# Optimization experiments

Hardware: AMD Instinct MI355X
Metric: run time of the kernel (lower is better)

## Reference

```python
import jax, jax.numpy as jnp
import numpy as np
import math

B, C, H, W = 64, 32, 80, 80
HEADS, HD = 8, 4
L = H * W
INV_PI = 1.0 / math.pi


def _conv2d(x, w, pad):
    return jax.lax.conv_general_dilated(x, w, (1, 1), pad, dimension_numbers=('NCHW', 'OIHW', 'NCHW'))


def _lin_angular(x, qkv_w, proj_w, proj_b, dconv_w):
    # x: (B, L, C) -> softmax-free angular linear attention
    qkv = (x @ qkv_w.T).reshape(B, L, 3, HEADS, HD).transpose(2, 0, 3, 1, 4)
    q, k, v = qkv[0], qkv[1], qkv[2]  # (B, HEADS, L, HD)
    q = q / jnp.linalg.norm(q, axis=-1, keepdims=True)
    k = k / jnp.linalg.norm(k, axis=-1, keepdims=True)
    # depthwise conv over L with kernel (9,1), one channel per head
    dconv_v = jax.lax.conv_general_dilated(v, dconv_w, (1, 1), ((4, 4), (0, 0)),
                                           feature_group_count=HEADS,
                                           dimension_numbers=('NCHW', 'OIHW', 'NCHW'))
    attn = jnp.einsum('bhld,bhle->bhde', k, v)  # (B,H,HD,HD)
    out = 0.5 * v + INV_PI * jnp.einsum('bhld,bhde->bhle', q, attn)
    out = out / jnp.linalg.norm(out, axis=-1, keepdims=True)
    out = out + dconv_v
    out = out.transpose(0, 2, 1, 3).reshape(B, L, C)
    return out @ proj_w.T + proj_b


def _xca(x, qkv_w, temp, proj_w, proj_b):
    # x: (B, L, C) -> cross-covariance (channel) attention
    qkv = (x @ qkv_w.T).reshape(B, L, 3, HEADS, HD).transpose(2, 0, 3, 4, 1)
    q, k, v = qkv[0], qkv[1], qkv[2]  # (B, HEADS, HD, L)
    q = q / jnp.maximum(jnp.linalg.norm(q, axis=-1, keepdims=True), 1e-12)
    k = k / jnp.maximum(jnp.linalg.norm(k, axis=-1, keepdims=True), 1e-12)
    attn = jax.nn.softmax(jnp.einsum('bhdn,bhen->bhde', q, k) * temp, axis=-1)
    out = jnp.einsum('bhde,bhen->bhdn', attn, v)  # (B,H,HD,L)
    out = out.transpose(0, 3, 1, 2).reshape(B, L, C)
    return out @ proj_w.T + proj_b


def _chan_vec(f, wa, ba, wa2, ba2, wm, bm, wm2, bm2):
    # f: (B, C, L) -> (B, C, 1) pooled channel descriptor (avg + max branches)
    avg = f.mean(axis=-1)  # (B, C)
    mx = f.max(axis=-1)    # (B, C)
    a = jax.nn.relu(avg @ wa.T + ba) @ wa2.T + ba2
    m = jax.nn.relu(mx @ wm.T + bm) @ wm2.T + bm2
    return (a + m)[..., None]  # (B, C, 1)


def _spatial_gate(a, c1w, c1b, c2w, c2b):
    # a: (B, C, L) -> (B, 1, L) softmax spatial gate
    am = a.reshape(B, C, H, W)
    pooled = jnp.concatenate([am.mean(axis=1, keepdims=True), am.max(axis=1, keepdims=True)], axis=1)
    y = jax.nn.relu(_conv2d(pooled, c1w, ((1, 1), (1, 1))) + c1b[None, :, None, None])
    y = _conv2d(y, c2w, ((1, 1), (1, 1))) + c2b[None, :, None, None]
    return jax.nn.softmax(y.reshape(B, 1, L), axis=-1)


def _forward(rgb, freq, la_qkv_w, la_proj_w, la_proj_b, la_dconv_w,
             xa_qkv_w, xa_temp, xa_proj_w, xa_proj_b,
             c1s_w, c1s_b, c2s_w, c2s_b,
             avg1_w, avg1_b, max1_w, max1_b, avg2_w, avg2_b, max2_w, max2_b,
             avg11_w, avg11_b, max11_w, max11_b, avg22_w, avg22_b, max22_w, max22_b):
    x1 = rgb.reshape(B, C, L).transpose(0, 2, 1)  # to_3d: (B, L, C)
    la1 = _lin_angular(x1, la_qkv_w, la_proj_w, la_proj_b, la_dconv_w)
    x2 = freq.reshape(B, C, L).transpose(0, 2, 1)
    xa1 = _xca(x2, xa_qkv_w, xa_temp, xa_proj_w, xa_proj_b)
    # CAFM works on flattened (B, C, L)
    f1 = la1.transpose(0, 2, 1)
    f2 = xa1.transpose(0, 2, 1)
    a1 = _chan_vec(f1, avg1_w, avg1_b, avg11_w, avg11_b, max1_w, max1_b, max11_w, max11_b)
    a2 = _chan_vec(f2, avg2_w, avg2_b, avg22_w, avg22_b, max2_w, max2_b, max22_w, max22_b)
    cross = jnp.einsum('bci,bdi->bcd', a1, a2)  # (B, C, C)
    a1f = jnp.einsum('bcd,bdl->bcl', jax.nn.softmax(cross, axis=-1), f1)
    a2f = jnp.einsum('bcd,bdl->bcl', jax.nn.softmax(cross.transpose(0, 2, 1), axis=-1), f2)
    g1 = _spatial_gate(a1f, c1s_w, c1s_b, c2s_w, c2s_b)
    g2 = _spatial_gate(a2f, c1s_w, c1s_b, c2s_w, c2s_b)
    f1 = f1 * g1 + f1
    f2 = f2 * g2 + f2
    # torch: (B,C,L).transpose(0,1) -> (C,B,L); sum; permute(1,2,0) -> (B,L,C); to_4d -> (B,C,H,W)
    # transposes cancel: equivalent to (f1+f2).reshape(B, C, H, W)
    return (f1 + f2).reshape(B, C, H, W)


def setup_inputs() -> dict:
    key = jax.random.key(0)
    ks = iter(jax.random.split(key, 40))
    def rn(shape, s=0.05):
        return jax.random.normal(next(ks), shape, dtype=jnp.float32) * s
    return dict(
        rgb=jax.random.normal(next(ks), (B, C, H, W), dtype=jnp.float32),
        freq=jax.random.normal(next(ks), (B, C, H, W), dtype=jnp.float32),
        la_qkv_w=rn((3 * C, C)), la_proj_w=rn((C, C)), la_proj_b=jnp.zeros((C,), jnp.float32),
        la_dconv_w=rn((HEADS, 1, 9, 1)),
        xa_qkv_w=rn((3 * C, C)), xa_temp=jnp.ones((HEADS, 1, 1), jnp.float32),
        xa_proj_w=rn((C, C)), xa_proj_b=jnp.zeros((C,), jnp.float32),
        c1s_w=rn((1, 2, 3, 3)), c1s_b=jnp.zeros((1,), jnp.float32),
        c2s_w=rn((1, 1, 3, 3)), c2s_b=jnp.zeros((1,), jnp.float32),
        avg1_w=rn((16, C)), avg1_b=jnp.zeros((16,), jnp.float32),
        max1_w=rn((16, C)), max1_b=jnp.zeros((16,), jnp.float32),
        avg2_w=rn((16, C)), avg2_b=jnp.zeros((16,), jnp.float32),
        max2_w=rn((16, C)), max2_b=jnp.zeros((16,), jnp.float32),
        avg11_w=rn((C, 16)), avg11_b=jnp.zeros((C,), jnp.float32),
        max11_w=rn((C, 16)), max11_b=jnp.zeros((C,), jnp.float32),
        avg22_w=rn((C, 16)), avg22_b=jnp.zeros((C,), jnp.float32),
        max22_w=rn((C, 16)), max22_b=jnp.zeros((C,), jnp.float32),
    )


def reference(rgb, freq, la_qkv_w, la_proj_w, la_proj_b, la_dconv_w,
              xa_qkv_w, xa_temp, xa_proj_w, xa_proj_b,
              c1s_w, c1s_b, c2s_w, c2s_b,
              avg1_w, avg1_b, max1_w, max1_b, avg2_w, avg2_b, max2_w, max2_b,
              avg11_w, avg11_b, max11_w, max11_b, avg22_w, avg22_b, max22_w, max22_b):
    return _forward(rgb, freq, la_qkv_w, la_proj_w, la_proj_b, la_dconv_w,
                    xa_qkv_w, xa_temp, xa_proj_w, xa_proj_b,
                    c1s_w, c1s_b, c2s_w, c2s_b,
                    avg1_w, avg1_b, max1_w, max1_b, avg2_w, avg2_b, max2_w, max2_b,
                    avg11_w, avg11_b, max11_w, max11_b, avg22_w, avg22_b, max22_w, max22_b)
```

## Files before the change

kernel.cpp:

```cpp
#include <hip/hip_runtime.h>

#define BN 64
#define CN 32
#define HEADSN 8
#define HDN 4
#define LN 6400
#define CL (CN*LN)


__device__ __forceinline__ unsigned fenc(float f){
  unsigned u = __float_as_uint(f);
  return (u & 0x80000000u) ? ~u : (u | 0x80000000u);
}
__device__ __forceinline__ float fdec(unsigned u){
  unsigned v = (u & 0x80000000u) ? (u & 0x7FFFFFFFu) : ~u;
  return __uint_as_float(v);
}

template<bool MAXOP>
__device__ __forceinline__ float bfly32(const float* in, int lane, int* chOut){
  const bool h0 = (lane & 1)  != 0, h1 = (lane & 2)  != 0, h2 = (lane & 4) != 0,
             h3 = (lane & 8)  != 0, h4 = (lane & 16) != 0;
  float a[16];
  #pragma unroll
  for (int i = 0; i < 16; ++i){
    float send = h0 ? in[i] : in[i+16];
    float keep = h0 ? in[i+16] : in[i];
    float recv = __shfl_xor(send, 1, 64);
    a[i] = MAXOP ? fmaxf(keep, recv) : keep + recv;
  }
  float b[8];
  #pragma unroll
  for (int i = 0; i < 8; ++i){
    float send = h1 ? a[i] : a[i+8];
    float keep = h1 ? a[i+8] : a[i];
    float recv = __shfl_xor(send, 2, 64);
    b[i] = MAXOP ? fmaxf(keep, recv) : keep + recv;
  }
  float c[4];
  #pragma unroll
  for (int i = 0; i < 4; ++i){
    float send = h2 ? b[i] : b[i+4];
    float keep = h2 ? b[i+4] : b[i];
    float recv = __shfl_xor(send, 4, 64);
    c[i] = MAXOP ? fmaxf(keep, recv) : keep + recv;
  }
  float d[2];
  #pragma unroll
  for (int i = 0; i < 2; ++i){
    float send = h3 ? c[i] : c[i+2];
    float keep = h3 ? c[i+2] : c[i];
    float recv = __shfl_xor(send, 8, 64);
    d[i] = MAXOP ? fmaxf(keep, recv) : keep + recv;
  }
  float e;
  {
    float send = h4 ? d[0] : d[1];
    float keep = h4 ? d[1] : d[0];
    float recv = __shfl_xor(send, 16, 64);
    e = MAXOP ? fmaxf(keep, recv) : keep + recv;
  }
  {
    float recv = __shfl_xor(e, 32, 64);
    e = MAXOP ? fmaxf(e, recv) : e + recv;
  }
  *chOut = (h0?16:0)|(h1?8:0)|(h2?4:0)|(h3?2:0)|(h4?1:0);
  return e;
}

__device__ __forceinline__ float bfly16_sum(const float* in, int lane, int* chOut){
  const bool h0 = (lane & 1) != 0, h1 = (lane & 2) != 0, h2 = (lane & 4) != 0,
             h3 = (lane & 8) != 0;
  float a[8];
  #pragma unroll
  for (int i = 0; i < 8; ++i){
    float send = h0 ? in[i] : in[i+8];
    float keep = h0 ? in[i+8] : in[i];
    float recv = __shfl_xor(send, 1, 64);
    a[i] = keep + recv;
  }
  float b[4];
  #pragma unroll
  for (int i = 0; i < 4; ++i){
    float send = h1 ? a[i] : a[i+4];
    float keep = h1 ? a[i+4] : a[i];
    float recv = __shfl_xor(send, 2, 64);
    b[i] = keep + recv;
  }
  float c[2];
  #pragma unroll
  for (int i = 0; i < 2; ++i){
    float send = h2 ? b[i] : b[i+2];
    float keep = h2 ? b[i+2] : b[i];
    float recv = __shfl_xor(send, 4, 64);
    c[i] = keep + recv;
  }
  float e;
  {
    float send = h3 ? c[0] : c[1];
    float keep = h3 ? c[1] : c[0];
    float recv = __shfl_xor(send, 8, 64);
    e = keep + recv;
  }
  e += __shfl_xor(e, 16, 64);
  e += __shfl_xor(e, 32, 64);
  *chOut = (h0?8:0)|(h1?4:0)|(h2?2:0)|(h3?1:0);
  return e;
}

__global__ __launch_bounds__(256, 4) void k_la_reduce(const float* __restrict__ rgb,
                                                      const float* __restrict__ Wqkv,
                                                      float* __restrict__ la_attn){
  __shared__ float2 xs2[256*17];
  const int b = blockIdx.y, l0 = blockIdx.x*256, tid = threadIdx.x;
  const float* xg = rgb + (size_t)b*CL + l0;
  #pragma unroll
  for (int c2 = 0; c2 < 16; ++c2){
    float e0 = xg[(2*c2)*LN + tid];
    float e1 = xg[(2*c2+1)*LN + tid];
    xs2[tid*17 + c2] = make_float2(e0, e1);
  }
  __syncthreads();
  const int wave = __builtin_amdgcn_readfirstlane(tid >> 6);
  const int lane = tid & 63;
  const float* Wk = Wqkv + (32 + wave*8)*32;
  const float* Wv = Wqkv + (64 + wave*8)*32;
  float acc[32];
  #pragma unroll
  for (int i = 0; i < 32; ++i) acc[i] = 0.f;
  for (int it = 0; it < 4; ++it){
    const int ll = it*64 + lane;
    float xv[32];
    #pragma unroll
    for (int c2 = 0; c2 < 16; ++c2){
      float2 t = xs2[ll*17 + c2];
      xv[2*c2] = t.x; xv[2*c2+1] = t.y;
    }
    float kk[8], vv[8];
    #pragma unroll
    for (int r = 0; r < 8; ++r){ kk[r] = 0.f; vv[r] = 0.f; }
    #pragma unroll
    for (int c = 0; c < 32; ++c){
      #pragma unroll
      for (int r = 0; r < 8; ++r){
        kk[r] = fmaf(Wk[r*32 + c], xv[c], kk[r]);
        vv[r] = fmaf(Wv[r*32 + c], xv[c], vv[r]);
      }
    }
    #pragma unroll
    for (int hh = 0; hh < 2; ++hh){
      const float* k = kk + hh*4;
      const float* v = vv + hh*4;
      float rn = rsqrtf(k[0]*k[0] + k[1]*k[1] + k[2]*k[2] + k[3]*k[3]);
      #pragma unroll
      for (int d = 0; d < 4; ++d){
        float kn = k[d]*rn;
        #pragma unroll
        for (int e = 0; e < 4; ++e)
          acc[hh*16 + d*4 + e] = fmaf(kn, v[e], acc[hh*16 + d*4 + e]);
      }
    }
  }
  int ch;
  float s = bfly32<false>(acc, lane, &ch);
  if (lane < 32) atomicAdd(la_attn + b*128 + wave*32 + ch, s);
}

__global__ __launch_bounds__(256, 4) void k_xa_reduce(const float* __restrict__ freq,
                                                      const float* __restrict__ Wqkv,
                                                      float* __restrict__ xa_sums){
  __shared__ float2 xs2[256*17];
  const int b = blockIdx.y, l0 = blockIdx.x*256, tid = threadIdx.x;
  const float* xg = freq + (size_t)b*CL + l0;
  #pragma unroll
  for (int c2 = 0; c2 < 16; ++c2){
    float e0 = xg[(2*c2)*LN + tid];
    float e1 = xg[(2*c2+1)*LN + tid];
    xs2[tid*17 + c2] = make_float2(e0, e1);
  }
  __syncthreads();
  const int wave = __builtin_amdgcn_readfirstlane(tid >> 6);
  const int lane = tid & 63;
  const float* Wq = Wqkv + (0  + wave*8)*32;
  const float* Wk = Wqkv + (32 + wave*8)*32;
  float acc[48];
  #pragma unroll
  for (int i = 0; i < 48; ++i) acc[i] = 0.f;
  for (int it = 0; it < 4; ++it){
    const int ll = it*64 + lane;
    float xv[32];
    #pragma unroll
    for (int c2 = 0; c2 < 16; ++c2){
      float2 t = xs2[ll*17 + c2];
      xv[2*c2] = t.x; xv[2*c2+1] = t.y;
    }
    float qq[8], kk[8];
    #pragma unroll
    for (int r = 0; r < 8; ++r){ qq[r] = 0.f; kk[r] = 0.f; }
    #pragma unroll
    for (int c = 0; c < 32; ++c){
      #pragma unroll
      for (int r = 0; r < 8; ++r){
        qq[r] = fmaf(Wq[r*32 + c], xv[c], qq[r]);
        kk[r] = fmaf(Wk[r*32 + c], xv[c], kk[r]);
      }
    }
    #pragma unroll
    for (int hh = 0; hh < 2; ++hh){
      const float* q = qq + hh*4;
      const float* k = kk + hh*4;
      const int base = hh*24;
      #pragma unroll
      for (int d = 0; d < 4; ++d){
        #pragma unroll
        for (int e = 0; e < 4; ++e)
          acc[base + d*4 + e] = fmaf(q[d], k[e], acc[base + d*4 + e]);
      }
      #pragma unroll
      for (int d = 0; d < 4; ++d) acc[base + 16 + d] = fmaf(q[d], q[d], acc[base + 16 + d]);
      #pragma unroll
      for (int e = 0; e < 4; ++e) acc[base + 20 + e] = fmaf(k[e], k[e], acc[base + 20 + e]);
    }
  }
  float* dst = xa_sums + b*192 + wave*48;
  int ch;
  float s0 = bfly32<false>(acc, lane, &ch);
  if (lane < 32) atomicAdd(dst + ch, s0);
  int ch2;
  float s1 = bfly16_sum(acc + 32, lane, &ch2);
  if (lane < 16) atomicAdd(dst + 32 + ch2, s1);
}

__global__ __launch_bounds__(64) void k_xa_soft(const float* __restrict__ xa_sums,
                                                const float* __restrict__ temp,
                                                float* __restrict__ xa_attn){
  const int b = blockIdx.x, t = threadIdx.x;
  if (t < 32){
    const int h = t >> 2, d = t & 3;
    const float* xss = xa_sums + b*192 + h*24;
    const float tmp = temp[h];
    const float nq = fmaxf(sqrtf(xss[16 + d]), 1e-12f);
    float lg[4]; float m = -1e30f;
    #pragma unroll
    for (int e = 0; e < 4; ++e){
      float nk = fmaxf(sqrtf(xss[20 + e]), 1e-12f);
      lg[e] = xss[d*4 + e] * tmp / (nq*nk);
      m = fmaxf(m, lg[e]);
    }
    float Z = 0.f;
    #pragma unroll
    for (int e = 0; e < 4; ++e){ lg[e] = __expf(lg[e] - m); Z += lg[e]; }
    float iZ = 1.f/Z;
    #pragma unroll
    for (int e = 0; e < 4; ++e) xa_attn[b*128 + h*16 + d*4 + e] = lg[e]*iZ;
  }
}

__global__ __launch_bounds__(256, 4) void k_la_final(const float* __restrict__ rgb,
    const float* __restrict__ Wqkv, const float* __restrict__ la_attn,
    const float* __restrict__ dconv_w, const float* __restrict__ Wp,
    const float* __restrict__ bp, float* __restrict__ f1,
    float* __restrict__ sum1, unsigned* __restrict__ max1e){
  __shared__ float2 vsh2[264*17];
  const int b = blockIdx.y, l0 = blockIdx.x*256, tid = threadIdx.x;
  const int l = l0 + tid, lane = tid & 63;
  const float* xg = rgb + (size_t)b*CL;
  float x[32];
  #pragma unroll
  for (int c = 0; c < 32; ++c) x[c] = xg[c*LN + l];
  {
    float v[32];
    #pragma unroll
    for (int r = 0; r < 32; ++r) v[r] = 0.f;
    const float* Wv = Wqkv + 64*32;
    #pragma unroll
    for (int c = 0; c < 32; ++c){
      #pragma unroll
      for (int r = 0; r < 32; ++r) v[r] = fmaf(Wv[r*32 + c], x[c], v[r]);
    }
    #pragma unroll
    for (int c2 = 0; c2 < 16; ++c2)
      vsh2[(tid+4)*17 + c2] = make_float2(v[2*c2], v[2*c2+1]);
  }
  if (tid < 128){
    const int p = tid >> 4, c2 = tid & 15;
    const int hl  = (p < 4) ? (l0 - 4 + p) : (l0 + 252 + p);
    const int pos = (p < 4) ? p : (256 + p);
    float2 vh = make_float2(0.f, 0.f);
    if (hl >= 0 && hl < LN){
      const float* W0 = Wqkv + (64 + 2*c2)*32;
      #pragma unroll 8
      for (int cc = 0; cc < 32; ++cc){
        float xv = xg[cc*LN + hl];
        vh.x = fmaf(W0[cc],      xv, vh.x);
        vh.y = fmaf(W0[32 + cc], xv, vh.y);
      }
    }
    vsh2[pos*17 + c2] = vh;
  }
  __syncthreads();
  float y[32];
  #pragma unroll
  for (int h = 0; h < 8; ++h){
    float q0 = 0.f, q1 = 0.f, q2 = 0.f, q3 = 0.f;
    const float* Wq = Wqkv + h*4*32;
    #pragma unroll
    for (int c = 0; c < 32; ++c){
      q0 = fmaf(Wq[c],      x[c], q0);
      q1 = fmaf(Wq[32 + c], x[c], q1);
      q2 = fmaf(Wq[64 + c], x[c], q2);
      q3 = fmaf(Wq[96 + c], x[c], q3);
    }
    const float rnq = rsqrtf(q0*q0 + q1*q1 + q2*q2 + q3*q3);
    q0 *= rnq; q1 *= rnq; q2 *= rnq; q3 *= rnq;
    const float* at = la_attn + b*128 + h*16;
    const float2 v01 = vsh2[(tid+4)*17 + h*2];
    const float2 v23 = vsh2[(tid+4)*17 + h*2 + 1];
    const float vo[4] = {v01.x, v01.y, v23.x, v23.y};
    float o[4]; float ss = 0.f;
    #pragma unroll
    for (int e = 0; e < 4; ++e){
      float t = 0.f;
      t = fmaf(q0, at[e],      t);
      t = fmaf(q1, at[4 + e],  t);
      t = fmaf(q2, at[8 + e],  t);
      t = fmaf(q3, at[12 + e], t);
      o[e] = fmaf(0.31830988618379067f, t, 0.5f*vo[e]);
      ss = fmaf(o[e], o[e], ss);
    }
    const float rno = rsqrtf(ss);
    float dc[4] = {0.f, 0.f, 0.f, 0.f};
    #pragma unroll
    for (int j = 0; j < 9; ++j){
      const float w = dconv_w[h*9 + j];
      const float2 p0 = vsh2[(tid + j)*17 + h*2];
      const float2 p1 = vsh2[(tid + j)*17 + h*2 + 1];
      dc[0] = fmaf(w, p0.x, dc[0]);
      dc[1] = fmaf(w, p0.y, dc[1]);
      dc[2] = fmaf(w, p1.x, dc[2]);
      dc[3] = fmaf(w, p1.y, dc[3]);
    }
    #pragma unroll
    for (int e = 0; e < 4; ++e) y[h*4 + e] = fmaf(o[e], rno, dc[e]);
  }
  float vals[32];
  float* f1p = f1 + (size_t)b*CL + l;
  #pragma unroll
  for (int r = 0; r < 32; ++r){
    float val = bp[r];
    #pragma unroll
    for (int c = 0; c < 32; ++c) val = fmaf(Wp[r*32 + c], y[c], val);
    f1p[r*LN] = val;
    vals[r] = val;
  }
  int ch;
  float s = bfly32<false>(vals, lane, &ch);
  float m = bfly32<true >(vals, lane, &ch);
  if (lane < 32){
    atomicAdd(&sum1[b*32 + ch], s);
    atomicMax(&max1e[b*32 + ch], fenc(m));
  }
}

__global__ __launch_bounds__(256, 4) void k_xa_final(const float* __restrict__ freq,
    const float* __restrict__ Wqkv, const float* __restrict__ xa_attn,
    const float* __restrict__ Wp, const float* __restrict__ bp,
    float* __restrict__ f2, float* __restrict__ sum2, unsigned* __restrict__ max2e){
  const int b = blockIdx.y, l0 = blockIdx.x*256, tid = threadIdx.x;
  const int l = l0 + tid, lane = tid & 63;
  const float* xg = freq + (size_t)b*CL;
  float x[32];
  #pragma unroll
  for (int c = 0; c < 32; ++c) x[c] = xg[c*LN + l];
  float v[32];
  #pragma unroll
  for (int r = 0; r < 32; ++r) v[r] = 0.f;
  const float* Wv = Wqkv + 64*32;
  #pragma unroll
  for (int c = 0; c < 32; ++c){
    #pragma unroll
    for (int r = 0; r < 32; ++r) v[r] = fmaf(Wv[r*32 + c], x[c], v[r]);
  }
  const float* at = xa_attn + b*128;
  float y[32];
  #pragma unroll
  for (int h = 0; h < 8; ++h){
    #pragma unroll
    for (int d = 0; d < 4; ++d){
      float t = 0.f;
      #pragma unroll
      for (int e = 0; e < 4; ++e) t = fmaf(at[h*16 + d*4 + e], v[h*4 + e], t);
      y[h*4 + d] = t;
    }
  }
  float vals[32];
  float* f2p = f2 + (size_t)b*CL + l;
  #pragma unroll
  for (int r = 0; r < 32; ++r){
    float val = bp[r];
    #pragma unroll
    for (int c = 0; c < 32; ++c) val = fmaf(Wp[r*32 + c], y[c], val);
    f2p[r*LN] = val;
    vals[r] = val;
  }
  int ch;
  float s = bfly32<false>(vals, lane, &ch);
  float m = bfly32<true >(vals, lane, &ch);
  if (lane < 32){
    atomicAdd(&sum2[b*32 + ch], s);
    atomicMax(&max2e[b*32 + ch], fenc(m));
  }
}

__global__ __launch_bounds__(64) void k_vec(
  const float* __restrict__ sum1, const unsigned* __restrict__ max1e,
  const float* __restrict__ sum2, const unsigned* __restrict__ max2e,
  const float* __restrict__ a1w, const float* __restrict__ a1b,
  const float* __restrict__ m1w, const float* __restrict__ m1b,
  const float* __restrict__ a2w, const float* __restrict__ a2b,
  const float* __restrict__ m2w, const float* __restrict__ m2b,
  const float* __restrict__ a11w, const float* __restrict__ a11b,
  const float* __restrict__ m11w, const float* __restrict__ m11b,
  const float* __restrict__ a22w, const float* __restrict__ a22b,
  const float* __restrict__ m22w, const float* __restrict__ m22b,
  float* __restrict__ w1o, float* __restrict__ w2o){
  __shared__ float avg1[32], mx1[32], avg2[32], mx2[32];
  __shared__ float h_a1[16], h_m1[16], h_a2[16], h_m2[16];
  __shared__ float a1v[32], a2v[32];
  const int b = blockIdx.x, t = threadIdx.x;
  if (t < 32){
    avg1[t] = sum1[b*32 + t] * (1.f/6400.f);
    mx1[t]  = fdec(max1e[b*32 + t]);
    avg2[t] = sum2[b*32 + t] * (1.f/6400.f);
    mx2[t]  = fdec(max2e[b*32 + t]);
  }
  __syncthreads();
  if (t < 16){
    float s1 = a1b[t], s2 = m1b[t], s3 = a2b[t], s4 = m2b[t];
    for (int c = 0; c < 32; ++c){
      s1 = fmaf(avg1[c], a1w[t*32 + c], s1);
      s2 = fmaf(mx1[c],  m1w[t*32 + c], s2);
      s3 = fmaf(avg2[c], a2w[t*32 + c], s3);
      s4 = fmaf(mx2[c],  m2w[t*32 + c], s4);
    }
    h_a1[t] = fmaxf(s1, 0.f); h_m1[t] = fmaxf(s2, 0.f);
    h_a2[t] = fmaxf(s3, 0.f); h_m2[t] = fmaxf(s4, 0.f);
  }
  __syncthreads();
  if (t < 32){
    float v1 = a11b[t] + m11b[t];
    float v2 = a22b[t] + m22b[t];
    for (int k = 0; k < 16; ++k){
      v1 += h_a1[k]*a11w[t*16 + k] + h_m1[k]*m11w[t*16 + k];
      v2 += h_a2[k]*a22w[t*16 + k] + h_m2[k]*m22w[t*16 + k];
    }
    a1v[t] = v1; a2v[t] = v2;
  }
  __syncthreads();
  if (t < 32){
    float s = a1v[t], m = -1e30f;
    for (int d = 0; d < 32; ++d) m = fmaxf(m, s*a2v[d]);
    float Z = 0.f;
    for (int d = 0; d < 32; ++d) Z += __expf(s*a2v[d] - m);
    float iZ = 1.f/Z;
    for (int d = 0; d < 32; ++d) w1o[b*1024 + t*32 + d] = __expf(s*a2v[d] - m)*iZ;
    float s2 = a2v[t]; m = -1e30f;
    for (int d = 0; d < 32; ++d) m = fmaxf(m, s2*a1v[d]);
    Z = 0.f;
    for (int d = 0; d < 32; ++d) Z += __expf(s2*a1v[d] - m);
    iZ = 1.f/Z;
    for (int d = 0; d < 32; ++d) w2o[b*1024 + t*32 + d] = __expf(s2*a1v[d] - m)*iZ;
  }
}

__global__ __launch_bounds__(256) void k_mix(const float* __restrict__ f1,
    const float* __restrict__ f2, const float* __restrict__ w1,
    const float* __restrict__ w2, float* __restrict__ pooled1,
    float* __restrict__ pooled2){
  const int b = blockIdx.y, l = blockIdx.x*256 + threadIdx.x;
  float fv[32];
  {
    const float* f1p = f1 + (size_t)b*CL + l;
    #pragma unroll
    for (int d = 0; d < 32; ++d) fv[d] = f1p[d*LN];
    const float* W = w1 + b*1024;
    float s = 0.f, m = -1e30f;
    #pragma unroll 8
    for (int c = 0; c < 32; ++c){
      float a = 0.f;
      #pragma unroll
      for (int d = 0; d < 32; ++d) a = fmaf(W[c*32 + d], fv[d], a);
      s += a; m = fmaxf(m, a);
    }
    pooled1[(size_t)b*2*LN + l]      = s*(1.f/32.f);
    pooled1[(size_t)b*2*LN + LN + l] = m;
  }
  {
    const float* f2p = f2 + (size_t)b*CL + l;
    #pragma unroll
    for (int d = 0; d < 32; ++d) fv[d] = f2p[d*LN];
    const float* W = w2 + b*1024;
    float s = 0.f, m = -1e30f;
    #pragma unroll 8
    for (int c = 0; c < 32; ++c){
      float a = 0.f;
      #pragma unroll
      for (int d = 0; d < 32; ++d) a = fmaf(W[c*32 + d], fv[d], a);
      s += a; m = fmaxf(m, a);
    }
    pooled2[(size_t)b*2*LN + l]      = s*(1.f/32.f);
    pooled2[(size_t)b*2*LN + LN + l] = m;
  }
}

__global__ __launch_bounds__(256) void k_gate(const float* __restrict__ pooled1,
    const float* __restrict__ pooled2, const float* __restrict__ c1w,
    const float* __restrict__ c1b, const float* __restrict__ c2w,
    const float* __restrict__ c2b, float* __restrict__ g1, float* __restrict__ g2){
  __shared__ float y1s[6400];
  __shared__ float red[8];
  const int b = blockIdx.y, t = blockIdx.x, tid = threadIdx.x;
  const float* src = (t == 0 ? pooled1 : pooled2) + (size_t)b*2*LN;
  float* dst = (t == 0 ? g1 : g2) + (size_t)b*LN;
  for (int i = tid; i < 6400; i += 256){
    const int yy = i/80, xx = i - yy*80;
    float a = c1b[0];
    #pragma unroll
    for (int ky = 0; ky < 3; ++ky){
      const int y2 = yy + ky - 1;
      if (y2 < 0 || y2 >= 80) continue;
      #pragma unroll
      for (int kx = 0; kx < 3; ++kx){
        const int x2 = xx + kx - 1;
        if (x2 < 0 || x2 >= 80) continue;
        const int j = y2*80 + x2;
        a = fmaf(src[j],        c1w[ky*3 + kx],     a);
        a = fmaf(src[6400 + j], c1w[9 + ky*3 + kx], a);
      }
    }
    y1s[i] = fmaxf(a, 0.f);
  }
  __syncthreads();
  float y2r[25]; float lmax = -1e30f;
  #pragma unroll
  for (int ii = 0; ii < 25; ++ii){
    const int i = tid + ii*256;
    const int yy = i/80, xx = i - yy*80;
    float a = c2b[0];
    #pragma unroll
    for (int ky = 0; ky < 3; ++ky){
      const int y2 = yy + ky - 1;
      if (y2 < 0 || y2 >= 80) continue;
      #pragma unroll
      for (int kx = 0; kx < 3; ++kx){
        const int x2 = xx + kx - 1;
        if (x2 < 0 || x2 >= 80) continue;
        a = fmaf(y1s[y2*80 + x2], c2w[ky*3 + kx], a);
      }
    }
    y2r[ii] = a; lmax = fmaxf(lmax, a);
  }
  #pragma unroll
  for (int off = 32; off >= 1; off >>= 1) lmax = fmaxf(lmax, __shfl_xor(lmax, off, 64));
  if ((tid & 63) == 0) red[tid >> 6] = lmax;
  __syncthreads();
  const float bmax = fmaxf(fmaxf(red[0], red[1]), fmaxf(red[2], red[3]));
  float lsum = 0.f;
  #pragma unroll
  for (int ii = 0; ii < 25; ++ii){
    float e = __expf(y2r[ii] - bmax);
    y2r[ii] = e; lsum += e;
  }
  #pragma unroll
  for (int off = 32; off >= 1; off >>= 1) lsum += __shfl_xor(lsum, off, 64);
  if ((tid & 63) == 0) red[4 + (tid >> 6)] = lsum;
  __syncthreads();
  const float inv = 1.f/(red[4] + red[5] + red[6] + red[7]);
  #pragma unroll
  for (int ii = 0; ii < 25; ++ii) dst[tid + ii*256] = y2r[ii]*inv;
}

__global__ __launch_bounds__(256) void k_final(const float* __restrict__ f1,
    const float* __restrict__ f2, const float* __restrict__ g1,
    const float* __restrict__ g2, float* __restrict__ out){
  const int i = blockIdx.x*256 + threadIdx.x;
  const int flat = i*4;
  const int b = flat / CL;
  const int rem = flat - b*CL;
  const int l = rem % LN;
  const float4 a  = *(const float4*)(f1 + flat);
  const float4 c  = *(const float4*)(f2 + flat);
  const float4 ga = *(const float4*)(g1 + b*LN + l);
  const float4 gc = *(const float4*)(g2 + b*LN + l);
  float4 o;
  o.x = fmaf(a.x, ga.x, a.x) + fmaf(c.x, gc.x, c.x);
  o.y = fmaf(a.y, ga.y, a.y) + fmaf(c.y, gc.y, c.y);
  o.z = fmaf(a.z, ga.z, a.z) + fmaf(c.z, gc.z, c.z);
  o.w = fmaf(a.w, ga.w, a.w) + fmaf(c.w, gc.w, c.w);
  *(float4*)(out + flat) = o;
}

extern "C" void kernel_launch(void* const* d_in, const int* in_sizes, int n_in,
                              void* d_out, int out_size, void* d_ws, size_t ws_size,
                              hipStream_t stream){
  const float* rgb     = (const float*)d_in[0];
  const float* freq    = (const float*)d_in[1];
  const float* la_qkv  = (const float*)d_in[2];
  const float* la_pw   = (const float*)d_in[3];
  const float* la_pb   = (const float*)d_in[4];
  const float* la_dw   = (const float*)d_in[5];
  const float* xa_qkv  = (const float*)d_in[6];
  const float* xa_temp = (const float*)d_in[7];
  const float* xa_pw   = (const float*)d_in[8];
  const float* xa_pb   = (const float*)d_in[9];
  const float* c1w     = (const float*)d_in[10];
  const float* c1b     = (const float*)d_in[11];
  const float* c2w     = (const float*)d_in[12];
  const float* c2b     = (const float*)d_in[13];

  float* ws = (float*)d_ws;
  size_t o = 0;
  float* f1      = ws + o; o += (size_t)BN*CL;
  float* f2      = ws + o; o += (size_t)BN*CL;
  float* la_attn = ws + o; o += BN*128;
  float* xa_sums = ws + o; o += BN*192;
  float* sum1    = ws + o; o += BN*32;
  unsigned* max1e = (unsigned*)(ws + o); o += BN*32;
  float* sum2    = ws + o; o += BN*32;
  unsigned* max2e = (unsigned*)(ws + o); o += BN*32;
  float* w1      = ws + o; o += BN*1024;
  float* w2      = ws + o; o += BN*1024;
  float* pooled1 = ws + o; o += (size_t)BN*2*LN;
  float* pooled2 = ws + o; o += (size_t)BN*2*LN;
  float* g1      = ws + o; o += (size_t)BN*LN;
  float* g2      = ws + o; o += (size_t)BN*LN;
  float* xa_attn = ws + o; o += BN*128;

  const size_t nz = (size_t)BN*128 + BN*192 + (size_t)BN*32*4;
  hipMemsetAsync(la_attn, 0, nz*sizeof(float), stream);

  k_la_reduce<<<dim3(25, BN), 256, 0, stream>>>(rgb, la_qkv, la_attn);
  k_xa_reduce<<<dim3(25, BN), 256, 0, stream>>>(freq, xa_qkv, xa_sums);
  k_xa_soft  <<<BN, 64, 0, stream>>>(xa_sums, xa_temp, xa_attn);
  k_la_final <<<dim3(25, BN), 256, 0, stream>>>(rgb, la_qkv, la_attn, la_dw, la_pw, la_pb,
                                                f1, sum1, max1e);
  k_xa_final <<<dim3(25, BN), 256, 0, stream>>>(freq, xa_qkv, xa_attn, xa_pw, xa_pb,
                                                f2, sum2, max2e);
  k_vec<<<BN, 64, 0, stream>>>(sum1, max1e, sum2, max2e,
      (const float*)d_in[14], (const float*)d_in[15], (const float*)d_in[16], (const float*)d_in[17],
      (const float*)d_in[18], (const float*)d_in[19], (const float*)d_in[20], (const float*)d_in[21],
      (const float*)d_in[22], (const float*)d_in[23], (const float*)d_in[24], (const float*)d_in[25],
      (const float*)d_in[26], (const float*)d_in[27], (const float*)d_in[28], (const float*)d_in[29],
      w1, w2);
  k_mix  <<<dim3(25, BN), 256, 0, stream>>>(f1, f2, w1, w2, pooled1, pooled2);
  k_gate <<<dim3(2, BN), 256, 0, stream>>>(pooled1, pooled2, c1w, c1b, c2w, c2b, g1, g2);
  k_final<<<12800, 256, 0, stream>>>(f1, f2, g1, g2, (float*)d_out);
}
```

Before: 579.6 us.

## Fold XCA attention and projection into per-batch matrix; restructure matvec loops

A new k_fold kernel computes per batch M2 = Wp · blockdiag(attn) · Wv, so k_xa_final does a single 32x32 matvec per pixel instead of a v projection, the attention mix and the output projection. In k_la_final, q and v are computed in one fused loop over x, and v is read from registers instead of shared memory. The output projections in k_la_final and k_mix are reordered to an outer-product loop over input channels, and k_mix gets an occupancy hint in its launch bounds. The changes cut FMA work and wasted loads, at the cost of more live registers (q and v both held in k_la_final) and a small extra launch-side fold.

```diff
diff --git a/kernel.cpp b/kernel.cpp
--- a/kernel.cpp
+++ b/kernel.cpp
@@ -231,9 +231,12 @@
   if (lane < 16) atomicAdd(dst + 32 + ch2, s1);
 }
 
-__global__ __launch_bounds__(64) void k_xa_soft(const float* __restrict__ xa_sums,
-                                                const float* __restrict__ temp,
-                                                float* __restrict__ xa_attn){
+__global__ __launch_bounds__(64) void k_fold(const float* __restrict__ xa_sums,
+                                             const float* __restrict__ temp,
+                                             const float* __restrict__ Wqkv,
+                                             const float* __restrict__ Wp,
+                                             float* __restrict__ M2){
+  __shared__ float attn_s[128];
   const int b = blockIdx.x, t = threadIdx.x;
   if (t < 32){
     const int h = t >> 2, d = t & 3;
@@ -252,7 +255,33 @@
     for (int e = 0; e < 4; ++e){ lg[e] = __expf(lg[e] - m); Z += lg[e]; }
     float iZ = 1.f/Z;
     #pragma unroll
-    for (int e = 0; e < 4; ++e) xa_attn[b*128 + h*16 + d*4 + e] = lg[e]*iZ;
+    for (int e = 0; e < 4; ++e) attn_s[h*16 + d*4 + e] = lg[e]*iZ;
+  }
+  __syncthreads();
+  if (t < 32){
+    const int c = t;
+    const float* Wv = Wqkv + 64*32;
+    float tmpv[32];
+    #pragma unroll
+    for (int k = 0; k < 32; ++k){
+      const int h = k >> 2, d = k & 3;
+      float s = 0.f;
+      #pragma unroll
+      for (int e = 0; e < 4; ++e)
+        s = fmaf(attn_s[h*16 + d*4 + e], Wv[(h*4 + e)*32 + c], s);
+      tmpv[k] = s;
+    }
+    float out[32];
+    #pragma unroll
+    for (int r = 0; r < 32; ++r) out[r] = 0.f;
+    #pragma unroll
+    for (int k = 0; k < 32; ++k){
+      #pragma unroll
+      for (int r = 0; r < 32; ++r)
+        out[r] = fmaf(Wp[r*32 + k], tmpv[k], out[r]);
+    }
+    #pragma unroll
+    for (int r = 0; r < 32; ++r) M2[b*1024 + r*32 + c] = out[r];
   }
 }
 
@@ -268,20 +297,24 @@
   float x[32];
   #pragma unroll
   for (int c = 0; c < 32; ++c) x[c] = xg[c*LN + l];
+  float v[32], q[32];
+  #pragma unroll
+  for (int r = 0; r < 32; ++r){ v[r] = 0.f; q[r] = 0.f; }
   {
-    float v[32];
-    #pragma unroll
-    for (int r = 0; r < 32; ++r) v[r] = 0.f;
+    const float* Wq = Wqkv;
     const float* Wv = Wqkv + 64*32;
     #pragma unroll
     for (int c = 0; c < 32; ++c){
       #pragma unroll
-      for (int r = 0; r < 32; ++r) v[r] = fmaf(Wv[r*32 + c], x[c], v[r]);
-    }
-    #pragma unroll
-    for (int c2 = 0; c2 < 16; ++c2)
-      vsh2[(tid+4)*17 + c2] = make_float2(v[2*c2], v[2*c2+1]);
-  }
+      for (int r = 0; r < 32; ++r){
+        v[r] = fmaf(Wv[r*32 + c], x[c], v[r]);
+        q[r] = fmaf(Wq[r*32 + c], x[c], q[r]);
+      }
+    }
+  }
+  #pragma unroll
+  for (int c2 = 0; c2 < 16; ++c2)
+    vsh2[(tid+4)*17 + c2] = make_float2(v[2*c2], v[2*c2+1]);
   if (tid < 128){
     const int p = tid >> 4, c2 = tid & 15;
     const int hl  = (p < 4) ? (l0 - 4 + p) : (l0 + 252 + p);
@@ -302,21 +335,10 @@
   float y[32];
   #pragma unroll
   for (int h = 0; h < 8; ++h){
-    float q0 = 0.f, q1 = 0.f, q2 = 0.f, q3 = 0.f;
-    const float* Wq = Wqkv + h*4*32;
-    #pragma unroll
-    for (int c = 0; c < 32; ++c){
-      q0 = fmaf(Wq[c],      x[c], q0);
-      q1 = fmaf(Wq[32 + c], x[c], q1);
-      q2 = fmaf(Wq[64 + c], x[c], q2);
-      q3 = fmaf(Wq[96 + c], x[c], q3);
-    }
+    float q0 = q[h*4], q1 = q[h*4+1], q2 = q[h*4+2], q3 = q[h*4+3];
     const float rnq = rsqrtf(q0*q0 + q1*q1 + q2*q2 + q3*q3);
     q0 *= rnq; q1 *= rnq; q2 *= rnq; q3 *= rnq;
     const float* at = la_attn + b*128 + h*16;
-    const float2 v01 = vsh2[(tid+4)*17 + h*2];
-    const float2 v23 = vsh2[(tid+4)*17 + h*2 + 1];
-    const float vo[4] = {v01.x, v01.y, v23.x, v23.y};
     float o[4]; float ss = 0.f;
     #pragma unroll
     for (int e = 0; e < 4; ++e){
@@ -325,7 +347,7 @@
       t = fmaf(q1, at[4 + e],  t);
       t = fmaf(q2, at[8 + e],  t);
       t = fmaf(q3, at[12 + e], t);
-      o[e] = fmaf(0.31830988618379067f, t, 0.5f*vo[e]);
+      o[e] = fmaf(0.31830988618379067f, t, 0.5f*v[h*4 + e]);
       ss = fmaf(o[e], o[e], ss);
     }
     const float rno = rsqrtf(ss);
@@ -344,15 +366,16 @@
     for (int e = 0; e < 4; ++e) y[h*4 + e] = fmaf(o[e], rno, dc[e]);
   }
   float vals[32];
+  #pragma unroll
+  for (int r = 0; r < 32; ++r) vals[r] = bp[r];
+  #pragma unroll
+  for (int c = 0; c < 32; ++c){
+    #pragma unroll
+    for (int r = 0; r < 32; ++r) vals[r] = fmaf(Wp[r*32 + c], y[c], vals[r]);
+  }
   float* f1p = f1 + (size_t)b*CL + l;
   #pragma unroll
-  for (int r = 0; r < 32; ++r){
-    float val = bp[r];
-    #pragma unroll
-    for (int c = 0; c < 32; ++c) val = fmaf(Wp[r*32 + c], y[c], val);
-    f1p[r*LN] = val;
-    vals[r] = val;
-  }
+  for (int r = 0; r < 32; ++r) f1p[r*LN] = vals[r];
   int ch;
   float s = bfly32<false>(vals, lane, &ch);
   float m = bfly32<true >(vals, lane, &ch);
@@ -363,8 +386,7 @@
 }
 
 __global__ __launch_bounds__(256, 4) void k_xa_final(const float* __restrict__ freq,
-    const float* __restrict__ Wqkv, const float* __restrict__ xa_attn,
-    const float* __restrict__ Wp, const float* __restrict__ bp,
+    const float* __restrict__ M2, const float* __restrict__ bp,
     float* __restrict__ f2, float* __restrict__ sum2, unsigned* __restrict__ max2e){
   const int b = blockIdx.y, l0 = blockIdx.x*256, tid = threadIdx.x;
   const int l = l0 + tid, lane = tid & 63;
@@ -372,37 +394,18 @@
   float x[32];
   #pragma unroll
   for (int c = 0; c < 32; ++c) x[c] = xg[c*LN + l];
-  float v[32];
-  #pragma unroll
-  for (int r = 0; r < 32; ++r) v[r] = 0.f;
-  const float* Wv = Wqkv + 64*32;
+  const float* M = M2 + b*1024;
+  float vals[32];
+  #pragma unroll
+  for (int r = 0; r < 32; ++r) vals[r] = bp[r];
   #pragma unroll
   for (int c = 0; c < 32; ++c){
     #pragma unroll
-    for (int r = 0; r < 32; ++r) v[r] = fmaf(Wv[r*32 + c], x[c], v[r]);
-  }
-  const float* at = xa_attn + b*128;
-  float y[32];
-  #pragma unroll
-  for (int h = 0; h < 8; ++h){
-    #pragma unroll
-    for (int d = 0; d < 4; ++d){
-      float t = 0.f;
-      #pragma unroll
-      for (int e = 0; e < 4; ++e) t = fmaf(at[h*16 + d*4 + e], v[h*4 + e], t);
-      y[h*4 + d] = t;
-    }
-  }
-  float vals[32];
+    for (int r = 0; r < 32; ++r) vals[r] = fmaf(M[r*32 + c], x[c], vals[r]);
+  }
   float* f2p = f2 + (size_t)b*CL + l;
   #pragma unroll
-  for (int r = 0; r < 32; ++r){
-    float val = bp[r];
-    #pragma unroll
-    for (int c = 0; c < 32; ++c) val = fmaf(Wp[r*32 + c], y[c], val);
-    f2p[r*LN] = val;
-    vals[r] = val;
-  }
+  for (int r = 0; r < 32; ++r) f2p[r*LN] = vals[r];
   int ch;
   float s = bfly32<false>(vals, lane, &ch);
   float m = bfly32<true >(vals, lane, &ch);
@@ -473,25 +476,27 @@
   }
 }
 
-__global__ __launch_bounds__(256) void k_mix(const float* __restrict__ f1,
+__global__ __launch_bounds__(256, 4) void k_mix(const float* __restrict__ f1,
     const float* __restrict__ f2, const float* __restrict__ w1,
     const float* __restrict__ w2, float* __restrict__ pooled1,
     float* __restrict__ pooled2){
   const int b = blockIdx.y, l = blockIdx.x*256 + threadIdx.x;
-  float fv[32];
+  float fv[32], av[32];
   {
     const float* f1p = f1 + (size_t)b*CL + l;
     #pragma unroll
     for (int d = 0; d < 32; ++d) fv[d] = f1p[d*LN];
     const float* W = w1 + b*1024;
+    #pragma unroll
+    for (int c = 0; c < 32; ++c) av[c] = 0.f;
+    #pragma unroll
+    for (int d = 0; d < 32; ++d){
+      #pragma unroll
+      for (int c = 0; c < 32; ++c) av[c] = fmaf(W[c*32 + d], fv[d], av[c]);
+    }
     float s = 0.f, m = -1e30f;
-    #pragma unroll 8
-    for (int c = 0; c < 32; ++c){
-      float a = 0.f;
-      #pragma unroll
-      for (int d = 0; d < 32; ++d) a = fmaf(W[c*32 + d], fv[d], a);
-      s += a; m = fmaxf(m, a);
-    }
+    #pragma unroll
+    for (int c = 0; c < 32; ++c){ s += av[c]; m = fmaxf(m, av[c]); }
     pooled1[(size_t)b*2*LN + l]      = s*(1.f/32.f);
     pooled1[(size_t)b*2*LN + LN + l] = m;
   }
@@ -500,14 +505,16 @@
     #pragma unroll
     for (int d = 0; d < 32; ++d) fv[d] = f2p[d*LN];
     const float* W = w2 + b*1024;
+    #pragma unroll
+    for (int c = 0; c < 32; ++c) av[c] = 0.f;
+    #pragma unroll
+    for (int d = 0; d < 32; ++d){
+      #pragma unroll
+      for (int c = 0; c < 32; ++c) av[c] = fmaf(W[c*32 + d], fv[d], av[c]);
+    }
     float s = 0.f, m = -1e30f;
-    #pragma unroll 8
-    for (int c = 0; c < 32; ++c){
-      float a = 0.f;
-      #pragma unroll
-      for (int d = 0; d < 32; ++d) a = fmaf(W[c*32 + d], fv[d], a);
-      s += a; m = fmaxf(m, a);
-    }
+    #pragma unroll
+    for (int c = 0; c < 32; ++c){ s += av[c]; m = fmaxf(m, av[c]); }
     pooled2[(size_t)b*2*LN + l]      = s*(1.f/32.f);
     pooled2[(size_t)b*2*LN + LN + l] = m;
   }
@@ -634,18 +641,17 @@
   float* pooled2 = ws + o; o += (size_t)BN*2*LN;
   float* g1      = ws + o; o += (size_t)BN*LN;
   float* g2      = ws + o; o += (size_t)BN*LN;
-  float* xa_attn = ws + o; o += BN*128;
+  float* M2      = ws + o; o += (size_t)BN*1024;
 
   const size_t nz = (size_t)BN*128 + BN*192 + (size_t)BN*32*4;
   hipMemsetAsync(la_attn, 0, nz*sizeof(float), stream);
 
   k_la_reduce<<<dim3(25, BN), 256, 0, stream>>>(rgb, la_qkv, la_attn);
   k_xa_reduce<<<dim3(25, BN), 256, 0, stream>>>(freq, xa_qkv, xa_sums);
-  k_xa_soft  <<<BN, 64, 0, stream>>>(xa_sums, xa_temp, xa_attn);
+  k_fold     <<<BN, 64, 0, stream>>>(xa_sums, xa_temp, xa_qkv, xa_pw, M2);
   k_la_final <<<dim3(25, BN), 256, 0, stream>>>(rgb, la_qkv, la_attn, la_dw, la_pw, la_pb,
                                                 f1, sum1, max1e);
-  k_xa_final <<<dim3(25, BN), 256, 0, stream>>>(freq, xa_qkv, xa_attn, xa_pw, xa_pb,
-                                                f2, sum2, max2e);
+  k_xa_final <<<dim3(25, BN), 256, 0, stream>>>(freq, M2, xa_pb, f2, sum2, max2e);
   k_vec<<<BN, 64, 0, stream>>>(sum1, max1e, sum2, max2e,
       (const float*)d_in[14], (const float*)d_in[15], (const float*)d_in[16], (const float*)d_in[17],
       (const float*)d_in[18], (const float*)d_in[19], (const float*)d_in[20], (const float*)d_in[21],
```

Result: slower. 921.8 us (+59.0%).
